# Kernel optimization log

Measured on AMD Instinct MI355X. Metric: run time of the kernel, lower is better.

The kernel has to match this reference:

```python
import jax, jax.numpy as jnp
import numpy as np

B, IN, OUT = 131072, 512, 512


def setup_inputs() -> dict:
    key = jax.random.key(0)
    k1, k2 = jax.random.split(key)
    x = jax.random.normal(k1, (B, IN), dtype=jnp.float32)
    # matches reset_parameters: normal(0, sqrt(1/in_features))
    weight = jax.random.normal(k2, (OUT, IN), dtype=jnp.float32) * jnp.sqrt(1.0 / IN)
    bias = jnp.zeros((OUT,), dtype=jnp.float32)
    return {"x": x, "weight": weight, "bias": bias}


def _binarize(w):
    # deterministic sign binarization: w >= 0 -> +1, else -1
    return jnp.where(w >= 0, 1.0, -1.0).astype(w.dtype)


def reference(x, weight, bias):
    wb = _binarize(weight)            # [out, in], values in {-1, +1}
    # out = x @ wb.T + bias           # [B, out]
    return jnp.einsum("bi,oi->bo", x, wb) + bias
```

## Files before the change

kernel.cpp:

```cpp
#include <hip/hip_runtime.h>
#include <stdint.h>


#define BATCH   131072
#define IN_F    512
#define OUT_F   512
#define BM      32
#define NCH     8
#define BUFB    8192

using f32x4  = __attribute__((ext_vector_type(4))) float;
using f32x16 = __attribute__((ext_vector_type(16))) float;
using short8 = __attribute__((ext_vector_type(8))) short;
using u32    = uint32_t;
using u64    = unsigned long long;

__global__ void prep_wbits(const float* __restrict__ W, u32* __restrict__ wp) {
    int t = blockIdx.x * blockDim.x + threadIdx.x;
    int l  = t & 63;
    int nf = t >> 6;
    const float* row = W + (size_t)(nf * 32 + (l & 31)) * IN_F + ((l >> 5) << 3);
#pragma unroll
    for (int q = 0; q < 8; ++q) {
        u32 word = 0;
#pragma unroll
        for (int b = 0; b < 4; ++b) {
            const float* p = row + (q * 4 + b) * 16;
            u32 by = 0;
#pragma unroll
            for (int j = 0; j < 8; ++j)
                by |= (p[j] >= 0.0f ? 0u : 1u) << j;
            word |= by << (8 * b);
        }
        wp[(size_t)t * 8 + q] = word;
    }
}

__device__ __forceinline__ short8 expB(u32 bb) {
    const u64 MUL = 0x1000200040008000ull;
    const u64 MSK = 0x8000800080008000ull;
    const u64 ONE = 0x3F803F803F803F80ull;
    u64 lo = ((u64)(bb & 0xFu) * MUL) & MSK;
    u64 hi = ((u64)((bb >> 4) & 0xFu) * MUL) & MSK;
    union { u64 d[2]; short8 v; } pk;
    pk.d[0] = ONE | lo;
    pk.d[1] = ONE | hi;
    return pk.v;
}

__global__ __launch_bounds__(512, 4) void gemm_bin(
    const float* __restrict__ X, const u32* __restrict__ WP,
    const float* __restrict__ bias, float* __restrict__ out) {

    __shared__ __align__(16) char smem[4 * BUFB];

    const int tid  = threadIdx.x;
    const int lane = tid & 63;
    const int wv   = tid >> 6;
    const int m0   = blockIdx.x * BM;
    const int col0 = wv * 64;

    const u32* wpp = WP + (((size_t)(wv * 2) * 64 + lane) << 3);
    uint4 a0 = *(const uint4*)(wpp);
    uint4 a1 = *(const uint4*)(wpp + 4);
    uint4 b0 = *(const uint4*)(wpp + 512);
    uint4 b1 = *(const uint4*)(wpp + 516);
    __builtin_amdgcn_sched_barrier(0);

    f32x16 acc[2];
#pragma unroll
    for (int fn = 0; fn < 2; ++fn) {
        const float bv = bias[col0 + fn * 32 + (lane & 31)];
#pragma unroll
        for (int r = 0; r < 16; ++r) acc[fn][r] = bv;
    }
    __builtin_amdgcn_sched_barrier(0);

    const u32 w0[8] = {a0.x, a0.y, a0.z, a0.w, a1.x, a1.y, a1.z, a1.w};
    const u32 w1[8] = {b0.x, b0.y, b0.z, b0.w, b1.x, b1.y, b1.z, b1.w};

    const int dr   = wv * 4 + (lane >> 4);
    const int ds4  = ((lane & 15) ^ (dr & 15)) << 2;
    const float* srcx = X + (size_t)(m0 + dr) * IN_F + ds4;

#define ISSUE_DMA(ck_)                                                         \
    {                                                                          \
        char* b_ = smem + ((ck_) & 3) * BUFB + wv * 1024;                      \
        __builtin_amdgcn_global_load_lds(                                      \
            (const __attribute__((address_space(1))) void*)(srcx + (ck_) * 64),\
            (__attribute__((address_space(3))) void*)(b_), 16, 0, 0);          \
    }

    ISSUE_DMA(0);
    ISSUE_DMA(1);
    ISSUE_DMA(2);
    __builtin_amdgcn_sched_barrier(0);

    const int arow = (lane & 31) * 256;
    const int aq32 = (lane >> 5) << 5;
    const int aswz = (lane & 15) << 4;

#pragma unroll
    for (int ck = 0; ck < NCH; ++ck) {
        short8 bf[4][2];
#pragma unroll
        for (int k4 = 0; k4 < 4; ++k4) {
            const int kt = ck * 4 + k4;
            bf[k4][0] = expB(w0[kt >> 2] >> ((kt & 3) * 8));
            bf[k4][1] = expB(w1[kt >> 2] >> ((kt & 3) * 8));
        }
        __builtin_amdgcn_sched_barrier(0);
        if (ck < NCH - 2)       asm volatile("s_waitcnt vmcnt(2)" ::: "memory");
        else if (ck == NCH - 2) asm volatile("s_waitcnt vmcnt(1)" ::: "memory");
        else                    asm volatile("s_waitcnt vmcnt(0)" ::: "memory");
        __builtin_amdgcn_sched_barrier(0);
        __builtin_amdgcn_s_barrier();
        __builtin_amdgcn_sched_barrier(0);
        if (ck + 3 < NCH) ISSUE_DMA(ck + 3);

        const char* ab = smem + (ck & 3) * BUFB;
#pragma unroll
        for (int k4 = 0; k4 < 4; ++k4) {
            const int blo = ((k4 << 6) + aq32) ^ aswz;
            f32x4 lo = *(const f32x4*)(ab + arow + blo);
            f32x4 hi = *(const f32x4*)(ab + arow + (blo ^ 16));
            u32 c0, c1, c2, c3;
            asm("v_cvt_pk_bf16_f32 %0, %1, %2" : "=v"(c0) : "v"(lo[0]), "v"(lo[1]));
            asm("v_cvt_pk_bf16_f32 %0, %1, %2" : "=v"(c1) : "v"(lo[2]), "v"(lo[3]));
            asm("v_cvt_pk_bf16_f32 %0, %1, %2" : "=v"(c2) : "v"(hi[0]), "v"(hi[1]));
            asm("v_cvt_pk_bf16_f32 %0, %1, %2" : "=v"(c3) : "v"(hi[2]), "v"(hi[3]));
            union { u32 w[4]; short8 v; } pk;
            pk.w[0] = c0; pk.w[1] = c1; pk.w[2] = c2; pk.w[3] = c3;
            __builtin_amdgcn_s_setprio(1);
            acc[0] = __builtin_amdgcn_mfma_f32_32x32x16_bf16(pk.v, bf[k4][0], acc[0], 0, 0, 0);
            acc[1] = __builtin_amdgcn_mfma_f32_32x32x16_bf16(pk.v, bf[k4][1], acc[1], 0, 0, 0);
            __builtin_amdgcn_s_setprio(0);
        }
    }
#undef ISSUE_DMA

    const int c     = lane & 31;
    const int rbase = (lane >> 5) << 2;
#pragma unroll
    for (int fn = 0; fn < 2; ++fn)
#pragma unroll
        for (int r = 0; r < 16; ++r) {
            const int row = (r & 3) + 8 * (r >> 2) + rbase;
            out[(size_t)(m0 + row) * OUT_F + col0 + fn * 32 + c] = acc[fn][r];
        }
}

extern "C" void kernel_launch(void* const* d_in, const int* in_sizes, int n_in,
                              void* d_out, int out_size, void* d_ws, size_t ws_size,
                              hipStream_t stream) {
    const float* X    = (const float*)d_in[0];
    const float* W    = (const float*)d_in[1];
    const float* bias = (const float*)d_in[2];
    float* o          = (float*)d_out;
    u32* wp           = (u32*)d_ws;

    hipLaunchKernelGGL(prep_wbits, dim3(4), dim3(256), 0, stream, W, wp);
    hipLaunchKernelGGL(gemm_bin, dim3(BATCH / BM), dim3(512), 0, stream,
                       X, wp, bias, o);
}
```

Baseline: 127.8 us.

## Double the block M tile to 64 rows with two row-groups per wave

Each block now computes 64 batch rows instead of 32. Each wave loads two 32-row A slices via LDS DMA and issues four MFMAs per k-step, reusing the expanded binary B fragments across both row groups. This halves the grid size and amortises per-block setup (the weight-bit loads and expansion) over twice as much work. In exchange it doubles LDS (64KB per block) and accumulator registers, which may lower occupancy below the launch-bounds target of 4 blocks.

```diff
diff --git a/kernel.cpp b/kernel.cpp
--- a/kernel.cpp
+++ b/kernel.cpp
@@ -5,9 +5,9 @@
 #define BATCH   131072
 #define IN_F    512
 #define OUT_F   512
-#define BM      32
+#define BM      64
 #define NCH     8
-#define BUFB    8192
+#define BUFB    16384
 
 using f32x4  = __attribute__((ext_vector_type(4))) float;
 using f32x16 = __attribute__((ext_vector_type(16))) float;
@@ -67,12 +67,14 @@
     uint4 b1 = *(const uint4*)(wpp + 516);
     __builtin_amdgcn_sched_barrier(0);
 
-    f32x16 acc[2];
+    f32x16 acc[2][2];
 #pragma unroll
     for (int fn = 0; fn < 2; ++fn) {
         const float bv = bias[col0 + fn * 32 + (lane & 31)];
 #pragma unroll
-        for (int r = 0; r < 16; ++r) acc[fn][r] = bv;
+        for (int rg = 0; rg < 2; ++rg)
+#pragma unroll
+            for (int r = 0; r < 16; ++r) acc[rg][fn][r] = bv;
     }
     __builtin_amdgcn_sched_barrier(0);
 
@@ -81,14 +83,18 @@
 
     const int dr   = wv * 4 + (lane >> 4);
     const int ds4  = ((lane & 15) ^ (dr & 15)) << 2;
-    const float* srcx = X + (size_t)(m0 + dr) * IN_F + ds4;
+    const float* src0 = X + (size_t)(m0 + dr) * IN_F + ds4;
+    const float* src1 = src0 + (size_t)32 * IN_F;
 
 #define ISSUE_DMA(ck_)                                                         \
     {                                                                          \
         char* b_ = smem + ((ck_) & 3) * BUFB + wv * 1024;                      \
         __builtin_amdgcn_global_load_lds(                                      \
-            (const __attribute__((address_space(1))) void*)(srcx + (ck_) * 64),\
+            (const __attribute__((address_space(1))) void*)(src0 + (ck_) * 64),\
             (__attribute__((address_space(3))) void*)(b_), 16, 0, 0);          \
+        __builtin_amdgcn_global_load_lds(                                      \
+            (const __attribute__((address_space(1))) void*)(src1 + (ck_) * 64),\
+            (__attribute__((address_space(3))) void*)(b_ + 8192), 16, 0, 0);   \
     }
 
     ISSUE_DMA(0);
@@ -110,8 +116,8 @@
             bf[k4][1] = expB(w1[kt >> 2] >> ((kt & 3) * 8));
         }
         __builtin_amdgcn_sched_barrier(0);
-        if (ck < NCH - 2)       asm volatile("s_waitcnt vmcnt(2)" ::: "memory");
-        else if (ck == NCH - 2) asm volatile("s_waitcnt vmcnt(1)" ::: "memory");
+        if (ck < NCH - 2)       asm volatile("s_waitcnt vmcnt(4)" ::: "memory");
+        else if (ck == NCH - 2) asm volatile("s_waitcnt vmcnt(2)" ::: "memory");
         else                    asm volatile("s_waitcnt vmcnt(0)" ::: "memory");
         __builtin_amdgcn_sched_barrier(0);
         __builtin_amdgcn_s_barrier();
@@ -122,18 +128,28 @@
 #pragma unroll
         for (int k4 = 0; k4 < 4; ++k4) {
             const int blo = ((k4 << 6) + aq32) ^ aswz;
-            f32x4 lo = *(const f32x4*)(ab + arow + blo);
-            f32x4 hi = *(const f32x4*)(ab + arow + (blo ^ 16));
-            u32 c0, c1, c2, c3;
-            asm("v_cvt_pk_bf16_f32 %0, %1, %2" : "=v"(c0) : "v"(lo[0]), "v"(lo[1]));
-            asm("v_cvt_pk_bf16_f32 %0, %1, %2" : "=v"(c1) : "v"(lo[2]), "v"(lo[3]));
-            asm("v_cvt_pk_bf16_f32 %0, %1, %2" : "=v"(c2) : "v"(hi[0]), "v"(hi[1]));
-            asm("v_cvt_pk_bf16_f32 %0, %1, %2" : "=v"(c3) : "v"(hi[2]), "v"(hi[3]));
-            union { u32 w[4]; short8 v; } pk;
-            pk.w[0] = c0; pk.w[1] = c1; pk.w[2] = c2; pk.w[3] = c3;
+            short8 afr[2];
+#pragma unroll
+            for (int rg = 0; rg < 2; ++rg) {
+                const char* p_ = ab + rg * 8192 + arow;
+                f32x4 lo = *(const f32x4*)(p_ + blo);
+                f32x4 hi = *(const f32x4*)(p_ + (blo ^ 16));
+                u32 c0, c1, c2, c3;
+                asm("v_cvt_pk_bf16_f32 %0, %1, %2" : "=v"(c0) : "v"(lo[0]), "v"(lo[1]));
+                asm("v_cvt_pk_bf16_f32 %0, %1, %2" : "=v"(c1) : "v"(lo[2]), "v"(lo[3]));
+                asm("v_cvt_pk_bf16_f32 %0, %1, %2" : "=v"(c2) : "v"(hi[0]), "v"(hi[1]));
+                asm("v_cvt_pk_bf16_f32 %0, %1, %2" : "=v"(c3) : "v"(hi[2]), "v"(hi[3]));
+                union { u32 w[4]; short8 v; } pk;
+                pk.w[0] = c0; pk.w[1] = c1; pk.w[2] = c2; pk.w[3] = c3;
+                afr[rg] = pk.v;
+            }
             __builtin_amdgcn_s_setprio(1);
-            acc[0] = __builtin_amdgcn_mfma_f32_32x32x16_bf16(pk.v, bf[k4][0], acc[0], 0, 0, 0);
-            acc[1] = __builtin_amdgcn_mfma_f32_32x32x16_bf16(pk.v, bf[k4][1], acc[1], 0, 0, 0);
+#pragma unroll
+            for (int rg = 0; rg < 2; ++rg)
+#pragma unroll
+                for (int fn = 0; fn < 2; ++fn)
+                    acc[rg][fn] = __builtin_amdgcn_mfma_f32_32x32x16_bf16(
+                        afr[rg], bf[k4][fn], acc[rg][fn], 0, 0, 0);
             __builtin_amdgcn_s_setprio(0);
         }
     }
@@ -142,12 +158,15 @@
     const int c     = lane & 31;
     const int rbase = (lane >> 5) << 2;
 #pragma unroll
-    for (int fn = 0; fn < 2; ++fn)
+    for (int rg = 0; rg < 2; ++rg)
 #pragma unroll
-        for (int r = 0; r < 16; ++r) {
-            const int row = (r & 3) + 8 * (r >> 2) + rbase;
-            out[(size_t)(m0 + row) * OUT_F + col0 + fn * 32 + c] = acc[fn][r];
-        }
+        for (int fn = 0; fn < 2; ++fn)
+#pragma unroll
+            for (int r = 0; r < 16; ++r) {
+                const int row = rg * 32 + (r & 3) + 8 * (r >> 2) + rbase;
+                out[(size_t)(m0 + row) * OUT_F + col0 + fn * 32 + c] =
+                    acc[rg][fn][r];
+            }
 }
 
 extern "C" void kernel_launch(void* const* d_in, const int* in_sizes, int n_in,
```

Result: slower. 437.9 us (+242.7%).
